# Kernel optimization log

Hardware: AMD Instinct MI355X
Metric: run time of the kernel (lower is better)

## Reference

```python
import jax, jax.numpy as jnp
import numpy as np

# config constants (from init_kwargs)
IMG_W = 800
IMG_H = 320
NUM_POINTS = 72
N_STRIPS = NUM_POINTS - 1
MAX_LANES = 4
REFINE_LAYERS = 3
CLS_W, REG_W, IOU_W = 2.0, 0.5, 2.0
ALPHA_NEG, ALPHA_POS, GAMMA = 0.1, 0.9, 2.0
LIOU_LEN = 15.0


def setup_inputs() -> dict:
    key = jax.random.key(0)
    k1, k2, k3, k4 = jax.random.split(key, 4)
    S, B, N, L, D = REFINE_LAYERS, 32, 2000, MAX_LANES, 2 + 4 + NUM_POINTS
    pred_fir = jax.random.uniform(k1, (S, B, N, D), dtype=jnp.float32)
    pred_sec = jax.random.uniform(k2, (S, B, N, D), dtype=jnp.float32)
    gt = jax.random.uniform(k3, (B, L, D), dtype=jnp.float32)
    gt = gt.at[..., 1].set(1.0)                    # all lanes valid
    # target offsets live in pixel coords; let some fall outside [0, IMG_W) to exercise invalid mask
    gt = gt.at[..., 6:].set(gt[..., 6:] * (IMG_W * 1.1) - 0.05 * IMG_W)
    diff = jax.random.uniform(k4, (S, N), dtype=jnp.float32)
    return {"predictions_fir": pred_fir, "predictions_sec": pred_sec,
            "gt_lane": gt, "diff": diff}


def _greedy_assign(cost):
    # cost: [N, L] -> matched prior row per target column, greedy without replacement
    N = cost.shape[0]
    def body(used, col):
        c = jnp.where(used, jnp.inf, col)
        r = jnp.argmin(c)
        return used.at[r].set(True), r
    _, rows = jax.lax.scan(body, jnp.zeros((N,), bool), cost.T)
    return rows  # [L] int32


def _assign_all(preds, gt):
    # preds: [S,B,N,D], gt: [B,L,D]; matching is under no_grad in the original
    p = jax.lax.stop_gradient(preds)
    t = jax.lax.stop_gradient(gt)
    score = jax.nn.softmax(p[..., :2], axis=-1)[..., 1]            # [S,B,N]
    geo = jnp.abs(p[..., :, None, 2:6] - t[None, :, None, :, 2:6]).sum(-1)   # [S,B,N,L]
    off = jnp.abs(p[..., :, None, 6:] - t[None, :, None, :, 6:] / (IMG_W - 1)).mean(-1)
    cost = geo + off - score[..., None]                            # [S,B,N,L]
    S, B, N, L = cost.shape
    rows = jax.vmap(_greedy_assign)(cost.reshape(S * B, N, L))
    return rows.reshape(S, B, L)


def _smooth_l1(d):
    ad = jnp.abs(d)
    return jnp.where(ad < 1.0, 0.5 * d * d, ad - 0.5)


def _branch_loss(preds, gt):
    # preds: [S,B,N,D], gt: [B,L,D] -> instance loss [N], last matched rows [L]
    S, B, N, _ = preds.shape
    L = gt.shape[1]
    rows = _assign_all(preds, gt)                                  # [S,B,L]

    # focal cls loss, per prior, summed over stages & batch
    cls_t = jax.nn.one_hot(rows, N, dtype=preds.dtype).sum(2)      # [S,B,N] 0/1
    logp = jax.nn.log_softmax(preds[..., :2], axis=-1)
    logpt = jnp.where(cls_t > 0, logp[..., 1], logp[..., 0])
    pt = jnp.exp(logpt)
    alpha_t = jnp.where(cls_t > 0, ALPHA_POS, ALPHA_NEG)
    cls_loss = (-alpha_t * (1.0 - pt) ** GAMMA * logpt).sum((0, 1)) / (B * REFINE_LAYERS)  # [N]

    # gather matched priors: [S,B,L,D]
    pm = jnp.take_along_axis(preds, rows[..., None], axis=2)
    tgt = gt[None]                                                 # [1,B,L,D]

    # smooth-L1 on (y, x, theta, length)
    sc = jnp.array([N_STRIPS, IMG_W - 1, 180.0, N_STRIPS], preds.dtype)
    d = pm[..., 2:6] * sc - tgt[..., 2:6] * sc
    reg_loss = (_smooth_l1(d).mean(-1) / L).sum((0, 1)) / (B * REFINE_LAYERS)  # [L]

    # line IoU loss on offsets
    rp = pm[..., 6:] * (IMG_W - 1)
    rt = jnp.broadcast_to(tgt[..., 6:], rp.shape)
    invalid = (rt < 0) | (rt >= IMG_W)
    ovr = jnp.minimum(rp + LIOU_LEN, rt + LIOU_LEN) - jnp.maximum(rp - LIOU_LEN, rt - LIOU_LEN)
    uni = jnp.maximum(rp + LIOU_LEN, rt + LIOU_LEN) - jnp.minimum(rp - LIOU_LEN, rt - LIOU_LEN)
    ovr = jnp.where(invalid, 0.0, ovr)
    uni = jnp.where(invalid, 0.0, uni)
    iou = ovr.sum(-1) / (uni.sum(-1) + 1e-9)                       # [S,B,L]
    iou_loss = ((1.0 - iou) / L).sum((0, 1)) / (B * REFINE_LAYERS) # [L]

    inst = cls_loss * CLS_W
    rows_last = rows[-1, -1]                                       # last stage, last image
    inst = inst.at[rows_last].add(reg_loss * REG_W + iou_loss * IOU_W)
    return inst


def reference(predictions_fir, predictions_sec, gt_lane, diff):
    loss_A = _branch_loss(predictions_fir, gt_lane)   # [N]
    loss_B = _branch_loss(predictions_sec, gt_lane)   # [N]
    diff_mean = diff.mean(0)                          # [N]
    delta = jax.lax.stop_gradient(jnp.median(loss_A - loss_B))
    loss_A = loss_A - delta / 2
    loss_B = loss_B + delta / 2
    total = jnp.sum((1.0 - diff_mean) * loss_A + diff_mean * loss_B)
    return total
```

## Files before the change

kernel.cpp:

```cpp
#include <hip/hip_runtime.h>
#include <math.h>

#define SDIM 3
#define BDIM 32
#define NPRI 2000
#define LDIM 4
#define DDIM 78
#define NSB (SDIM * BDIM)


__global__ __launch_bounds__(1024) void fused_kernel(
    const float* __restrict__ predsA, const float* __restrict__ predsB,
    const float* __restrict__ gt,
    int* __restrict__ rowsws, float* __restrict__ regacc,
    float* __restrict__ corrws, float* __restrict__ clsSum)
{
    const int sb = blockIdx.x, branch = blockIdx.y;
    const float* preds = branch ? predsB : predsA;
    const int bimg = sb % BDIM;
    const int tid = threadIdx.x;
    const int wv = tid >> 6, lane = tid & 63;

    __shared__ float cost[LDIM][NPRI];
    __shared__ float tg[36 * 8];
    __shared__ float geo4[16];
    __shared__ float redv[16];
    __shared__ int   redi[16];
    __shared__ int   rows_lds[LDIM];

    {
        const float* gtb = gt + (size_t)bimg * LDIM * DDIM;
        if (tid < 288) {
            int jj = tid >> 3, t = tid & 7, l = t >> 1, k = t & 1;
            tg[tid] = gtb[l * DDIM + 6 + 2 * jj + k] / 799.0f;
        }
        if (tid < 16) geo4[tid] = gtb[(tid >> 2) * DDIM + 2 + (tid & 3)];
    }
    __syncthreads();

    const int h = tid & 3;
    const float* gpb = preds + (size_t)sb * NPRI * DDIM;

    for (int pass = 0; pass < 8; ++pass) {
        const int n = pass * 256 + (tid >> 2);
        if (n < NPRI) {
            const float* p = gpb + (size_t)n * DDIM;
            float2 hd0 = *(const float2*)(p);
            float2 hd1 = *(const float2*)(p + 2);
            float2 hd2 = *(const float2*)(p + 4);
            const float2* pb = (const float2*)(p + 6 + h * 18);
            float2 ov[9];
#pragma unroll
            for (int q = 0; q < 9; ++q) ov[q] = pb[q];

            float offs0 = 0.f, offs1 = 0.f, offs2 = 0.f, offs3 = 0.f;
#pragma unroll
            for (int q = 0; q < 9; ++q) {
                float pv0 = ov[q].x;
                float pv1 = ov[q].y;
                const float4* t4 = (const float4*)(tg + (h * 9 + q) * 8);
                float4 ta = t4[0], tb = t4[1];
                offs0 += fabsf(pv0 - ta.x); offs0 += fabsf(pv1 - ta.y);
                offs1 += fabsf(pv0 - ta.z); offs1 += fabsf(pv1 - ta.w);
                offs2 += fabsf(pv0 - tb.x); offs2 += fabsf(pv1 - tb.y);
                offs3 += fabsf(pv0 - tb.z); offs3 += fabsf(pv1 - tb.w);
            }
            offs0 += __shfl_xor(offs0, 1); offs1 += __shfl_xor(offs1, 1);
            offs2 += __shfl_xor(offs2, 1); offs3 += __shfl_xor(offs3, 1);
            offs0 += __shfl_xor(offs0, 2); offs1 += __shfl_xor(offs1, 2);
            offs2 += __shfl_xor(offs2, 2); offs3 += __shfl_xor(offs3, 2);

            float a = hd0.x, b1 = hd0.y;
            float m = fmaxf(a, b1);
            float ea = expf(a - m), eb = expf(b1 - m);
            float score = eb / (ea + eb);
            float g0 = hd1.x, g1 = hd1.y, g2 = hd2.x, g3 = hd2.y;

            float mo01 = (h & 1) ? offs1 : offs0;
            float mo23 = (h & 1) ? offs3 : offs2;
            float myoffs = (h & 2) ? mo23 : mo01;

            float geo = fabsf(g0 - geo4[h * 4 + 0]) + fabsf(g1 - geo4[h * 4 + 1])
                      + fabsf(g2 - geo4[h * 4 + 2]) + fabsf(g3 - geo4[h * 4 + 3]);
            cost[h][n] = geo + myoffs / 72.0f - score;

            if (h == 0) {
                float lse = m + logf(ea + eb);
                float logpt = a - lse;
                float pt = expf(logpt);
                float om = 1.0f - pt;
                atomicAdd(&clsSum[branch * NPRI + n], -(0.1f * om * om * logpt));
            }
        }
    }
    __syncthreads();

    for (int l = 0; l < LDIM; ++l) {
        float bv = INFINITY; int bi = 0x7fffffff;
        for (int k = tid; k < NPRI; k += 1024) {
            float v = cost[l][k];
            if (v < bv) { bv = v; bi = k; }
        }
#pragma unroll
        for (int off = 32; off > 0; off >>= 1) {
            float v2 = __shfl_down(bv, off);
            int   i2 = __shfl_down(bi, off);
            if (v2 < bv || (v2 == bv && i2 < bi)) { bv = v2; bi = i2; }
        }
        if (lane == 0) { redv[wv] = bv; redi[wv] = bi; }
        __syncthreads();
        if (tid == 0) {
            float fv = redv[0]; int fi = redi[0];
#pragma unroll
            for (int w = 1; w < 16; ++w)
                if (redv[w] < fv || (redv[w] == fv && redi[w] < fi)) { fv = redv[w]; fi = redi[w]; }
            rows_lds[l] = fi;
            cost[0][fi] = INFINITY; cost[1][fi] = INFINITY;
            cost[2][fi] = INFINITY; cost[3][fi] = INFINITY;
        }
        __syncthreads();
    }
    if (tid < LDIM && sb == NSB - 1) rowsws[branch * LDIM + tid] = rows_lds[tid];

    if (wv < 4) {
        const int l = wv;
        const int row = rows_lds[l];
        const float* pm = preds + ((size_t)sb * NPRI + row) * DDIM;
        const float* tgp = gt + ((size_t)bimg * LDIM + l) * DDIM;

        float osum = 0.f, usum = 0.f, rterm = 0.f;
        {
            float rp = pm[6 + lane] * 799.0f;
            float rt = tgp[6 + lane];
            bool inv = (rt < 0.0f) || (rt >= 800.0f);
            float ov = fminf(rp, rt) - fmaxf(rp, rt) + 30.0f;
            float un = fmaxf(rp, rt) - fminf(rp, rt) + 30.0f;
            if (!inv) { osum += ov; usum += un; }
        }
        if (lane < 8) {
            float rp = pm[6 + lane + 64] * 799.0f;
            float rt = tgp[6 + lane + 64];
            bool inv = (rt < 0.0f) || (rt >= 800.0f);
            float ov = fminf(rp, rt) - fmaxf(rp, rt) + 30.0f;
            float un = fmaxf(rp, rt) - fminf(rp, rt) + 30.0f;
            if (!inv) { osum += ov; usum += un; }
        }
        if (lane < 4) {
            const float scv[4] = {71.0f, 799.0f, 180.0f, 71.0f};
            float s = scv[lane];
            float d = pm[2 + lane] * s - tgp[2 + lane] * s;
            float ad = fabsf(d);
            rterm = (ad < 1.0f) ? 0.5f * d * d : ad - 0.5f;
        }
#pragma unroll
        for (int off = 32; off > 0; off >>= 1) {
            osum += __shfl_down(osum, off);
            usum += __shfl_down(usum, off);
            rterm += __shfl_down(rterm, off);
        }
        if (lane == 0) {
            float iou = osum / (usum + 1e-9f);
            atomicAdd(&regacc[branch * 8 + l], (rterm / 4.0f) / 4.0f);
            atomicAdd(&regacc[branch * 8 + 4 + l], (1.0f - iou) / 4.0f);

            float a = pm[0], b1 = pm[1];
            float m = fmaxf(a, b1);
            float ea = expf(a - m), eb = expf(b1 - m);
            float lse = m + logf(ea + eb);
            float lp0 = a - lse, lp1 = b1 - lse;
            float pt0 = expf(lp0), pt1 = expf(lp1);
            float om0 = 1.0f - pt0, om1 = 1.0f - pt1;
            float neg = -(0.1f * om0 * om0 * lp0);
            float pos = -(0.9f * om1 * om1 * lp1);
            atomicAdd(&corrws[branch * NPRI + row], pos - neg);
        }
    }
}

__global__ __launch_bounds__(1024) void final_kernel(
    const float* __restrict__ clsSum, const float* __restrict__ corrws,
    const float* __restrict__ regacc, const int* __restrict__ rowsws,
    const float* __restrict__ diff, float* __restrict__ out)
{
    __shared__ float instA[NPRI];
    __shared__ float instB[NPRI];
    __shared__ float sbuf[2048];
    __shared__ float red[1024];
    const int tid = threadIdx.x;

    for (int n = tid; n < NPRI; n += 1024) {
        float ia = (clsSum[n] + corrws[n]) * (2.0f / 96.0f);
        float ib = (clsSum[NPRI + n] + corrws[NPRI + n]) * (2.0f / 96.0f);
#pragma unroll
        for (int l = 0; l < 4; ++l) {
            if (rowsws[l] == n)
                ia += (regacc[l] / 96.0f) * 0.5f + (regacc[4 + l] / 96.0f) * 2.0f;
            if (rowsws[4 + l] == n)
                ib += (regacc[8 + l] / 96.0f) * 0.5f + (regacc[12 + l] / 96.0f) * 2.0f;
        }
        instA[n] = ia; instB[n] = ib;
        sbuf[n] = ia - ib;
    }
    if (tid < 2048 - NPRI) sbuf[NPRI + tid] = INFINITY;
    __syncthreads();

    for (int k = 2; k <= 2048; k <<= 1) {
        for (int j = k >> 1; j > 0; j >>= 1) {
            for (int i = tid; i < 2048; i += 1024) {
                int ixj = i ^ j;
                if (ixj > i) {
                    bool up = ((i & k) == 0);
                    float x = sbuf[i], y = sbuf[ixj];
                    if ((x > y) == up) { sbuf[i] = y; sbuf[ixj] = x; }
                }
            }
            __syncthreads();
        }
    }
    float delta = 0.5f * (sbuf[999] + sbuf[1000]);

    float acc = 0.0f;
    for (int n = tid; n < NPRI; n += 1024) {
        float dm = (diff[n] + diff[NPRI + n] + diff[2 * NPRI + n]) / 3.0f;
        acc += (1.0f - dm) * (instA[n] - 0.5f * delta)
             + dm * (instB[n] + 0.5f * delta);
    }
    red[tid] = acc;
    __syncthreads();
    for (int s = 512; s > 0; s >>= 1) {
        if (tid < s) red[tid] += red[tid + s];
        __syncthreads();
    }
    if (tid == 0) out[0] = red[0];
}

extern "C" void kernel_launch(void* const* d_in, const int* in_sizes, int n_in,
                              void* d_out, int out_size, void* d_ws, size_t ws_size,
                              hipStream_t stream)
{
    const float* predsA = (const float*)d_in[0];
    const float* predsB = (const float*)d_in[1];
    const float* gt     = (const float*)d_in[2];
    const float* diff   = (const float*)d_in[3];
    float* out = (float*)d_out;

    int*   rowsws = (int*)d_ws;
    float* clsSum = (float*)(rowsws + 8);
    float* corrws = clsSum + 2 * NPRI;
    float* regacc = corrws + 2 * NPRI;

    hipMemsetAsync(clsSum, 0, (4 * NPRI + 16) * sizeof(float), stream);

    dim3 g1(NSB, 2);
    fused_kernel<<<g1, 1024, 0, stream>>>(predsA, predsB, gt,
                                          rowsws, regacc, corrws, clsSum);

    final_kernel<<<1, 1024, 0, stream>>>(clsSum, corrws, regacc, rowsws, diff, out);
}
```

Baseline: 187.3 us.

## Replace bitonic median sort with radix select; double-buffer prior loads in cost pass

The final kernel no longer bitonic-sorts all 2048 differences to find the median. It maps the floats to order-preserving unsigned keys and runs a 4-round 8-bit radix select to find the 999th element, then uses a count/min reduction to get the 1000th. This cuts the many barrier-separated sort stages down to a few histogram rounds. The fused kernel also software-pipelines the per-prior global loads across two register buffers, so the next prior's loads are in flight while the current one is computed. That raises register pressure at 1024 threads per block.

```diff
diff --git a/kernel.cpp b/kernel.cpp
--- a/kernel.cpp
+++ b/kernel.cpp
@@ -39,58 +39,74 @@
     __syncthreads();
 
     const int h = tid & 3;
+    const int nid = tid >> 2;
     const float* gpb = preds + (size_t)sb * NPRI * DDIM;
 
-    for (int pass = 0; pass < 8; ++pass) {
-        const int n = pass * 256 + (tid >> 2);
-        if (n < NPRI) {
-            const float* p = gpb + (size_t)n * DDIM;
-            float2 hd0 = *(const float2*)(p);
-            float2 hd1 = *(const float2*)(p + 2);
-            float2 hd2 = *(const float2*)(p + 4);
-            const float2* pb = (const float2*)(p + 6 + h * 18);
-            float2 ov[9];
-#pragma unroll
-            for (int q = 0; q < 9; ++q) ov[q] = pb[q];
-
-            float offs0 = 0.f, offs1 = 0.f, offs2 = 0.f, offs3 = 0.f;
-#pragma unroll
-            for (int q = 0; q < 9; ++q) {
-                float pv0 = ov[q].x;
-                float pv1 = ov[q].y;
-                const float4* t4 = (const float4*)(tg + (h * 9 + q) * 8);
-                float4 ta = t4[0], tb = t4[1];
-                offs0 += fabsf(pv0 - ta.x); offs0 += fabsf(pv1 - ta.y);
-                offs1 += fabsf(pv0 - ta.z); offs1 += fabsf(pv1 - ta.w);
-                offs2 += fabsf(pv0 - tb.x); offs2 += fabsf(pv1 - tb.y);
-                offs3 += fabsf(pv0 - tb.z); offs3 += fabsf(pv1 - tb.w);
-            }
-            offs0 += __shfl_xor(offs0, 1); offs1 += __shfl_xor(offs1, 1);
-            offs2 += __shfl_xor(offs2, 1); offs3 += __shfl_xor(offs3, 1);
-            offs0 += __shfl_xor(offs0, 2); offs1 += __shfl_xor(offs1, 2);
-            offs2 += __shfl_xor(offs2, 2); offs3 += __shfl_xor(offs3, 2);
-
-            float a = hd0.x, b1 = hd0.y;
-            float m = fmaxf(a, b1);
-            float ea = expf(a - m), eb = expf(b1 - m);
-            float score = eb / (ea + eb);
-            float g0 = hd1.x, g1 = hd1.y, g2 = hd2.x, g3 = hd2.y;
-
-            float mo01 = (h & 1) ? offs1 : offs0;
-            float mo23 = (h & 1) ? offs3 : offs2;
-            float myoffs = (h & 2) ? mo23 : mo01;
-
-            float geo = fabsf(g0 - geo4[h * 4 + 0]) + fabsf(g1 - geo4[h * 4 + 1])
-                      + fabsf(g2 - geo4[h * 4 + 2]) + fabsf(g3 - geo4[h * 4 + 3]);
-            cost[h][n] = geo + myoffs / 72.0f - score;
-
-            if (h == 0) {
-                float lse = m + logf(ea + eb);
-                float logpt = a - lse;
-                float pt = expf(logpt);
-                float om = 1.0f - pt;
-                atomicAdd(&clsSum[branch * NPRI + n], -(0.1f * om * om * logpt));
-            }
+    auto loadp = [&](int nn, float2& h0, float2& h1, float2& h2, float2 (&ov)[9]) {
+        const float* p = gpb + (size_t)nn * DDIM;
+        h0 = *(const float2*)(p);
+        h1 = *(const float2*)(p + 2);
+        h2 = *(const float2*)(p + 4);
+        const float2* pb = (const float2*)(p + 6 + h * 18);
+#pragma unroll
+        for (int q = 0; q < 9; ++q) ov[q] = pb[q];
+    };
+    auto computep = [&](int nn, float2 hd0, float2 hd1, float2 hd2,
+                        const float2 (&ov)[9]) {
+        float offs0 = 0.f, offs1 = 0.f, offs2 = 0.f, offs3 = 0.f;
+#pragma unroll
+        for (int q = 0; q < 9; ++q) {
+            float pv0 = ov[q].x;
+            float pv1 = ov[q].y;
+            const float4* t4 = (const float4*)(tg + (h * 9 + q) * 8);
+            float4 ta = t4[0], tb = t4[1];
+            offs0 += fabsf(pv0 - ta.x); offs0 += fabsf(pv1 - ta.y);
+            offs1 += fabsf(pv0 - ta.z); offs1 += fabsf(pv1 - ta.w);
+            offs2 += fabsf(pv0 - tb.x); offs2 += fabsf(pv1 - tb.y);
+            offs3 += fabsf(pv0 - tb.z); offs3 += fabsf(pv1 - tb.w);
+        }
+        offs0 += __shfl_xor(offs0, 1); offs1 += __shfl_xor(offs1, 1);
+        offs2 += __shfl_xor(offs2, 1); offs3 += __shfl_xor(offs3, 1);
+        offs0 += __shfl_xor(offs0, 2); offs1 += __shfl_xor(offs1, 2);
+        offs2 += __shfl_xor(offs2, 2); offs3 += __shfl_xor(offs3, 2);
+
+        float a = hd0.x, b1 = hd0.y;
+        float m = fmaxf(a, b1);
+        float ea = expf(a - m), eb = expf(b1 - m);
+        float score = eb / (ea + eb);
+        float g0 = hd1.x, g1 = hd1.y, g2 = hd2.x, g3 = hd2.y;
+
+        float mo01 = (h & 1) ? offs1 : offs0;
+        float mo23 = (h & 1) ? offs3 : offs2;
+        float myoffs = (h & 2) ? mo23 : mo01;
+
+        float geo = fabsf(g0 - geo4[h * 4 + 0]) + fabsf(g1 - geo4[h * 4 + 1])
+                  + fabsf(g2 - geo4[h * 4 + 2]) + fabsf(g3 - geo4[h * 4 + 3]);
+        cost[h][nn] = geo + myoffs / 72.0f - score;
+
+        if (h == 0) {
+            float lse = m + logf(ea + eb);
+            float logpt = a - lse;
+            float pt = expf(logpt);
+            float om = 1.0f - pt;
+            atomicAdd(&clsSum[branch * NPRI + nn], -(0.1f * om * om * logpt));
+        }
+    };
+
+    {
+        float2 hA0, hA1, hA2, hB0, hB1, hB2;
+        float2 ovA[9], ovB[9];
+        int nA = nid;
+        if (nA < NPRI) loadp(nA, hA0, hA1, hA2, ovA);
+#pragma unroll
+        for (int pp = 0; pp < 4; ++pp) {
+            const int nB = (2 * pp + 1) * 256 + nid;
+            if (nB < NPRI) loadp(nB, hB0, hB1, hB2, ovB);
+            if (nA < NPRI) computep(nA, hA0, hA1, hA2, ovA);
+            const int nA2 = (2 * pp + 2) * 256 + nid;
+            if (pp < 3 && nA2 < NPRI) loadp(nA2, hA0, hA1, hA2, ovA);
+            if (nB < NPRI) computep(nB, hB0, hB1, hB2, ovB);
+            nA = nA2;
         }
     }
     __syncthreads();
@@ -177,6 +193,15 @@
     }
 }
 
+__device__ __forceinline__ unsigned mapf(float f) {
+    unsigned u = __float_as_uint(f);
+    return (u & 0x80000000u) ? ~u : (u | 0x80000000u);
+}
+__device__ __forceinline__ float unmapf(unsigned u) {
+    return (u & 0x80000000u) ? __uint_as_float(u ^ 0x80000000u)
+                             : __uint_as_float(~u);
+}
+
 __global__ __launch_bounds__(1024) void final_kernel(
     const float* __restrict__ clsSum, const float* __restrict__ corrws,
     const float* __restrict__ regacc, const int* __restrict__ rowsws,
@@ -184,9 +209,18 @@
 {
     __shared__ float instA[NPRI];
     __shared__ float instB[NPRI];
-    __shared__ float sbuf[2048];
-    __shared__ float red[1024];
+    __shared__ unsigned keys[NPRI];
+    __shared__ unsigned bufA[NPRI];
+    __shared__ unsigned bufB[NPRI];
+    __shared__ unsigned cnt[256];
+    __shared__ unsigned wpre[4];
+    __shared__ unsigned selBin, selBefore, outCnt;
+    __shared__ int      redc[16];
+    __shared__ unsigned redm[16];
+    __shared__ float    deltaSh;
+    __shared__ float    red[1024];
     const int tid = threadIdx.x;
+    const int wv = tid >> 6, lane = tid & 63;
 
     for (int n = tid; n < NPRI; n += 1024) {
         float ia = (clsSum[n] + corrws[n]) * (2.0f / 96.0f);
@@ -199,25 +233,91 @@
                 ib += (regacc[8 + l] / 96.0f) * 0.5f + (regacc[12 + l] / 96.0f) * 2.0f;
         }
         instA[n] = ia; instB[n] = ib;
-        sbuf[n] = ia - ib;
-    }
-    if (tid < 2048 - NPRI) sbuf[NPRI + tid] = INFINITY;
+        keys[n] = mapf(ia - ib);
+    }
     __syncthreads();
 
-    for (int k = 2; k <= 2048; k <<= 1) {
-        for (int j = k >> 1; j > 0; j >>= 1) {
-            for (int i = tid; i < 2048; i += 1024) {
-                int ixj = i ^ j;
-                if (ixj > i) {
-                    bool up = ((i & k) == 0);
-                    float x = sbuf[i], y = sbuf[ixj];
-                    if ((x > y) == up) { sbuf[i] = y; sbuf[ixj] = x; }
+    int curk = 999;
+    unsigned prefix = 0;
+    unsigned m = NPRI;
+    unsigned* src = keys;
+    unsigned* dst = bufA;
+
+    for (int r = 0; r < 4; ++r) {
+        const int shift = 24 - 8 * r;
+        if (tid < 256) cnt[tid] = 0;
+        __syncthreads();
+        for (unsigned i = tid; i < m; i += 1024)
+            atomicAdd(&cnt[(src[i] >> shift) & 255u], 1u);
+        __syncthreads();
+
+        unsigned v = 0, inc = 0;
+        if (tid < 256) {
+            v = cnt[tid]; inc = v;
+#pragma unroll
+            for (int o = 1; o < 64; o <<= 1) {
+                unsigned t = __shfl_up(inc, o);
+                if ((tid & 63) >= o) inc += t;
+            }
+            if ((tid & 63) == 63) wpre[tid >> 6] = inc;
+        }
+        __syncthreads();
+        if (tid < 256) {
+            unsigned base = 0;
+#pragma unroll
+            for (int w = 0; w < 3; ++w) if (w < (tid >> 6)) base += wpre[w];
+            unsigned incl = base + inc, excl = incl - v;
+            if (v > 0 && (unsigned)curk >= excl && (unsigned)curk < incl) {
+                selBin = tid; selBefore = excl;
+            }
+        }
+        __syncthreads();
+        const unsigned b = selBin;
+        curk -= (int)selBefore;
+        prefix |= b << shift;
+
+        if (r < 3) {
+            if (tid == 0) outCnt = 0;
+            __syncthreads();
+            for (unsigned i = tid; i < m; i += 1024) {
+                unsigned u = src[i];
+                if (((u >> shift) & 255u) == b) {
+                    unsigned p = atomicAdd(&outCnt, 1u);
+                    dst[p] = u;
                 }
             }
             __syncthreads();
-        }
-    }
-    float delta = 0.5f * (sbuf[999] + sbuf[1000]);
+            m = outCnt;
+            src = dst;
+            dst = (dst == bufA) ? bufB : bufA;
+        }
+    }
+    const unsigned v999u = prefix;
+
+    {
+        int cle = 0; unsigned mn = 0xffffffffu;
+        for (int j = tid; j < NPRI; j += 1024) {
+            unsigned u = keys[j];
+            cle += (u <= v999u);
+            if (u > v999u) mn = min(mn, u);
+        }
+#pragma unroll
+        for (int off = 32; off > 0; off >>= 1) {
+            cle += __shfl_down(cle, off);
+            mn = min(mn, (unsigned)__shfl_down(mn, off));
+        }
+        if (lane == 0) { redc[wv] = cle; redm[wv] = mn; }
+        __syncthreads();
+        if (tid == 0) {
+            int c = 0; unsigned m2 = 0xffffffffu;
+#pragma unroll
+            for (int w = 0; w < 16; ++w) { c += redc[w]; m2 = min(m2, redm[w]); }
+            unsigned v1000u = (c >= 1001) ? v999u : m2;
+            deltaSh = 0.5f * (unmapf(v999u) + unmapf(v1000u));
+        }
+        __syncthreads();
+    }
+    const float delta = deltaSh;
 
     float acc = 0.0f;
     for (int n = tid; n < NPRI; n += 1024) {
```

After: 175.7 us. -6.1%, faster.
